# Kernel tuning notes

Measured on AMD Instinct MI355X. Metric: run time of the kernel, lower is better.

## Reference

```python
import jax, jax.numpy as jnp
import numpy as np

B, T = 16, 256
SD, AD = 24, 8
K = SD + AD           # in_dim
H = 1                 # num_heads
HD1, HD2 = 256, 256


def setup_inputs() -> dict:
    key = jax.random.key(0)
    ks = jax.random.split(key, 16)
    p = lambda kk, shp, s=0.05: jax.random.normal(kk, shp, dtype=jnp.float32) * s
    inp = {
        "state": jax.random.normal(ks[0], (B, T, SD), dtype=jnp.float32),
        "action": jax.random.normal(ks[1], (B, T, AD), dtype=jnp.float32),
        "Wq": p(ks[2], (H * K, K)), "bq": p(ks[3], (H * K,)),
        "Wk": p(ks[4], (H * K, K)), "bk": p(ks[5], (H * K,)),
        "Wv": p(ks[6], (H * K, K)), "bv": p(ks[7], (H * K,)),
        "W1": p(ks[8], (HD1, H * K + K)), "b1": p(ks[9], (HD1,)),
        "W2": p(ks[10], (HD2, HD1)), "b2": p(ks[11], (HD2,)),
        # out layer init_layer_uniform(-0.003, 0.003)
        "Wout": jax.random.uniform(ks[12], (1, HD1), minval=-0.003, maxval=0.003, dtype=jnp.float32),
        "bout": jax.random.uniform(ks[13], (1,), minval=-0.003, maxval=0.003, dtype=jnp.float32),
    }
    return inp


def reference(state, action, Wq, bq, Wk, bk, Wv, bv, W1, b1, W2, b2, Wout, bout):
    s = jnp.concatenate([state, action], axis=-1)            # (b,t,k)
    b, t, k = s.shape
    h = H
    # rel[b,i,j,:] = s[b,j] - s[b,i]
    rel = s[:, None, :, :] - s[:, :, None, :]                # (b,t,t,k)
    q = jax.nn.relu(jnp.einsum('btk,nk->btn', s, Wq) + bq).reshape(b, t, h, k)
    kk = jax.nn.relu(jnp.einsum('bijk,nk->bijn', rel, Wk) + bk).reshape(b, t, t, h, k)
    vv = jax.nn.relu(jnp.einsum('bijk,nk->bijn', rel, Wv) + bv).reshape(b, t, t, h, k)
    scores = jnp.einsum('bijhk,bihk->bhij', kk, q) / jnp.sqrt(jnp.float32(k))
    w = jax.nn.softmax(scores, axis=-1)                      # softmax over j
    x = jnp.einsum('bhij,bijhk->bihk', w, vv).reshape(b, t, h * k)
    x = jnp.concatenate([x, s], axis=-1)                     # (b,t,h*k+k)
    x = jax.nn.relu(jnp.einsum('btn,mn->btm', x, W1) + b1)
    x = jax.nn.relu(jnp.einsum('btn,mn->btm', x, W2) + b2)
    value = jnp.einsum('btn,mn->btm', x, Wout) + bout        # (b,t,1)
    return value
```

## Files before the change

kernel.cpp:

```cpp
#include <hip/hip_runtime.h>

#define NB 16
#define NT 256
#define NK 32
#define NROWS (NB * NT)
static constexpr float INV_SQRT_K = 0.17677669529663687f;

__global__ __launch_bounds__(256) void prep_kernel(
    const float* __restrict__ state, const float* __restrict__ action,
    const float* __restrict__ Wq, const float* __restrict__ bq,
    const float* __restrict__ Wk, const float* __restrict__ Wv,
    float* __restrict__ q, float* __restrict__ Ks, float* __restrict__ Vs,
    float* __restrict__ xcat)
{
    __shared__ float s_sh[8][32];
    const int tid = threadIdx.x;
    const int r = tid >> 5, n = tid & 31;
    const int row = blockIdx.x * 8 + r;
    float sval = (n < 24) ? state[row * 24 + n] : action[row * 8 + (n - 24)];
    s_sh[r][n] = sval;
    __syncthreads();
    float aq = 0.f, ak = 0.f, av = 0.f;
#pragma unroll
    for (int k = 0; k < 32; ++k) {
        float sv = s_sh[r][k];
        aq = fmaf(sv, Wq[n * 32 + k], aq);
        ak = fmaf(sv, Wk[n * 32 + k], ak);
        av = fmaf(sv, Wv[n * 32 + k], av);
    }
    q[row * 32 + n]  = fmaxf(aq + bq[n], 0.f);
    Ks[row * 32 + n] = ak;
    Vs[row * 32 + n] = av;
    xcat[row * 64 + 32 + n] = sval;
}

__global__ __launch_bounds__(256) void attn_kernel(
    const float* __restrict__ q, const float* __restrict__ Ks,
    const float* __restrict__ Vs, const float* __restrict__ bk,
    const float* __restrict__ bv, float* __restrict__ xcat)
{
    __shared__ float Ki[32], Vi[32], qi[32], bks[32], bvs[32];
    __shared__ float sc[256];
    __shared__ float wred[4];
    __shared__ float part[8][32];
    const int tid = threadIdx.x;
    const int b = blockIdx.x >> 8, i = blockIdx.x & 255;
    const int ibase = (b * 256 + i) * 32;
    if (tid < 32) {
        Ki[tid]  = Ks[ibase + tid];
        Vi[tid]  = Vs[ibase + tid];
        qi[tid]  = q[ibase + tid];
        bks[tid] = bk[tid];
        bvs[tid] = bv[tid];
    }
    __syncthreads();

    const int j = tid;
    const float* kp = Ks + (b * 256 + j) * 32;
    float acc = 0.f;
#pragma unroll
    for (int k = 0; k < 32; ++k) {
        float kkv = fmaxf(kp[k] - Ki[k] + bks[k], 0.f);
        acc = fmaf(kkv, qi[k], acc);
    }
    const float sval = acc * INV_SQRT_K;

    float m = sval;
#pragma unroll
    for (int off = 32; off >= 1; off >>= 1) m = fmaxf(m, __shfl_xor(m, off));
    if ((tid & 63) == 0) wred[tid >> 6] = m;
    __syncthreads();
    m = fmaxf(fmaxf(wred[0], wred[1]), fmaxf(wred[2], wred[3]));
    const float e = expf(sval - m);
    float ssum = e;
#pragma unroll
    for (int off = 32; off >= 1; off >>= 1) ssum += __shfl_xor(ssum, off);
    __syncthreads();
    if ((tid & 63) == 0) wred[tid >> 6] = ssum;
    __syncthreads();
    const float tot = (wred[0] + wred[1]) + (wred[2] + wred[3]);
    sc[j] = e / tot;
    __syncthreads();

    const int k = tid & 31, g = tid >> 5;
    const float* vp = Vs + (b * 256 + g * 32) * 32;
    const float vi = Vi[k], bvk = bvs[k];
    float xacc = 0.f;
#pragma unroll
    for (int jj = 0; jj < 32; ++jj) {
        float vv = fmaxf(vp[jj * 32 + k] - vi + bvk, 0.f);
        xacc = fmaf(sc[g * 32 + jj], vv, xacc);
    }
    part[g][k] = xacc;
    __syncthreads();
    if (tid < 32) {
        float x = 0.f;
#pragma unroll
        for (int gg = 0; gg < 8; ++gg) x += part[gg][tid];
        xcat[(b * 256 + i) * 64 + tid] = x;
    }
}

__global__ __launch_bounds__(256) void mlp_kernel(
    const float* __restrict__ xcat,
    const float* __restrict__ W1, const float* __restrict__ b1,
    const float* __restrict__ W2, const float* __restrict__ b2,
    const float* __restrict__ Wout, const float* __restrict__ bout,
    float* __restrict__ out)
{
    __shared__ float xc[8][64];
    __shared__ float h1[8][256];
    __shared__ float h2[8][256];
    const int tid = threadIdx.x;
    const int row0 = blockIdx.x * 8;

    ((float*)xc)[tid]       = xcat[row0 * 64 + tid];
    ((float*)xc)[tid + 256] = xcat[row0 * 64 + tid + 256];
    __syncthreads();

    const int m = tid;
    float acc[8];
#pragma unroll
    for (int r = 0; r < 8; ++r) acc[r] = 0.f;
    const float* w1p = W1 + m * 64;
#pragma unroll 8
    for (int n = 0; n < 64; ++n) {
        float w = w1p[n];
#pragma unroll
        for (int r = 0; r < 8; ++r) acc[r] = fmaf(w, xc[r][n], acc[r]);
    }
    float bb = b1[m];
#pragma unroll
    for (int r = 0; r < 8; ++r) h1[r][m] = fmaxf(acc[r] + bb, 0.f);
    __syncthreads();

#pragma unroll
    for (int r = 0; r < 8; ++r) acc[r] = 0.f;
    const float* w2p = W2 + m * 256;
#pragma unroll 4
    for (int n = 0; n < 256; ++n) {
        float w = w2p[n];
#pragma unroll
        for (int r = 0; r < 8; ++r) acc[r] = fmaf(w, h1[r][n], acc[r]);
    }
    bb = b2[m];
#pragma unroll
    for (int r = 0; r < 8; ++r) h2[r][m] = fmaxf(acc[r] + bb, 0.f);
    __syncthreads();

    if (tid < 128) {
        const int r = tid >> 4, l = tid & 15;
        float a = 0.f;
        for (int n = l; n < 256; n += 16) a = fmaf(h2[r][n], Wout[n], a);
#pragma unroll
        for (int mm = 8; mm >= 1; mm >>= 1) a += __shfl_xor(a, mm);
        if (l == 0) out[row0 + r] = a + bout[0];
    }
}

extern "C" void kernel_launch(void* const* d_in, const int* in_sizes, int n_in,
                              void* d_out, int out_size, void* d_ws, size_t ws_size,
                              hipStream_t stream)
{
    const float* state  = (const float*)d_in[0];
    const float* action = (const float*)d_in[1];
    const float* Wq     = (const float*)d_in[2];
    const float* bq     = (const float*)d_in[3];
    const float* Wk     = (const float*)d_in[4];
    const float* bk     = (const float*)d_in[5];
    const float* Wv     = (const float*)d_in[6];
    const float* bv     = (const float*)d_in[7];
    const float* W1     = (const float*)d_in[8];
    const float* b1     = (const float*)d_in[9];
    const float* W2     = (const float*)d_in[10];
    const float* b2     = (const float*)d_in[11];
    const float* Wout   = (const float*)d_in[12];
    const float* bout   = (const float*)d_in[13];
    float* out = (float*)d_out;

    float* ws   = (float*)d_ws;
    float* q    = ws;
    float* Ks   = q  + NROWS * NK;
    float* Vs   = Ks + NROWS * NK;
    float* xcat = Vs + NROWS * NK;

    prep_kernel<<<NROWS / 8, 256, 0, stream>>>(state, action, Wq, bq, Wk, Wv,
                                               q, Ks, Vs, xcat);
    attn_kernel<<<NROWS, 256, 0, stream>>>(q, Ks, Vs, bk, bv, xcat);
    mlp_kernel<<<NROWS / 8, 256, 0, stream>>>(xcat, W1, b1, W2, b2, Wout, bout, out);
}
```

Before: 134.2 us.

## Process four query rows per attention block and fold biases into projections

The attention kernel now handles four query rows i per block, so each j-row of K and V loaded from global memory is reused across four queries. K rows are loaded with float4 into registers. The bias terms and the 1/sqrt(k) scale move into the prep kernel, which removes per-element adds in the inner loops. The softmax is restructured so each wave reduces one query row with shuffles only, dropping several block barriers. This uses more registers and shared memory per block and launches a quarter as many blocks.

```diff
diff --git a/kernel.cpp b/kernel.cpp
--- a/kernel.cpp
+++ b/kernel.cpp
@@ -4,13 +4,15 @@
 #define NT 256
 #define NK 32
 #define NROWS (NB * NT)
+#define GQ 4
 static constexpr float INV_SQRT_K = 0.17677669529663687f;
 
 __global__ __launch_bounds__(256) void prep_kernel(
     const float* __restrict__ state, const float* __restrict__ action,
     const float* __restrict__ Wq, const float* __restrict__ bq,
-    const float* __restrict__ Wk, const float* __restrict__ Wv,
-    float* __restrict__ q, float* __restrict__ Ks, float* __restrict__ Vs,
+    const float* __restrict__ Wk, const float* __restrict__ bk,
+    const float* __restrict__ Wv, const float* __restrict__ bv,
+    float* __restrict__ q, float* __restrict__ Ksb, float* __restrict__ Vsb,
     float* __restrict__ xcat)
 {
     __shared__ float s_sh[8][32];
@@ -28,76 +30,100 @@
         ak = fmaf(sv, Wk[n * 32 + k], ak);
         av = fmaf(sv, Wv[n * 32 + k], av);
     }
-    q[row * 32 + n]  = fmaxf(aq + bq[n], 0.f);
-    Ks[row * 32 + n] = ak;
-    Vs[row * 32 + n] = av;
+    q[row * 32 + n]   = fmaxf(aq + bq[n], 0.f) * INV_SQRT_K;
+    Ksb[row * 32 + n] = ak + bk[n];
+    Vsb[row * 32 + n] = av + bv[n];
     xcat[row * 64 + 32 + n] = sval;
 }
 
 __global__ __launch_bounds__(256) void attn_kernel(
-    const float* __restrict__ q, const float* __restrict__ Ks,
-    const float* __restrict__ Vs, const float* __restrict__ bk,
+    const float* __restrict__ q, const float* __restrict__ Ksb,
+    const float* __restrict__ Vsb, const float* __restrict__ bk,
     const float* __restrict__ bv, float* __restrict__ xcat)
 {
-    __shared__ float Ki[32], Vi[32], qi[32], bks[32], bvs[32];
-    __shared__ float sc[256];
-    __shared__ float wred[4];
-    __shared__ float part[8][32];
+    __shared__ float Kie[GQ][32];
+    __shared__ float Vie[GQ][32];
+    __shared__ float qi[GQ][32];
+    __shared__ float sc[GQ][256];
+    __shared__ float part[GQ][8][32];
     const int tid = threadIdx.x;
-    const int b = blockIdx.x >> 8, i = blockIdx.x & 255;
-    const int ibase = (b * 256 + i) * 32;
-    if (tid < 32) {
-        Ki[tid]  = Ks[ibase + tid];
-        Vi[tid]  = Vs[ibase + tid];
-        qi[tid]  = q[ibase + tid];
-        bks[tid] = bk[tid];
-        bvs[tid] = bv[tid];
+    const int b  = blockIdx.x >> 6;
+    const int i0 = (blockIdx.x & 63) << 2;
+    const int rowbase = b * 256;
+
+    {
+        const int g = (tid >> 5) & 3, k = tid & 31;
+        const int ib = (rowbase + i0 + g) * 32 + k;
+        if (tid < 128) {
+            Kie[g][k] = Ksb[ib] - bk[k];
+            qi[g][k]  = q[ib];
+        } else {
+            Vie[g][k] = Vsb[ib] - bv[k];
+        }
     }
     __syncthreads();
 
     const int j = tid;
-    const float* kp = Ks + (b * 256 + j) * 32;
-    float acc = 0.f;
+    const float4* kp4 = (const float4*)(Ksb + (rowbase + j) * 32);
+    float kr[32];
+#pragma unroll
+    for (int u = 0; u < 8; ++u) {
+        float4 v = kp4[u];
+        kr[u * 4 + 0] = v.x; kr[u * 4 + 1] = v.y;
+        kr[u * 4 + 2] = v.z; kr[u * 4 + 3] = v.w;
+    }
+    float acc[GQ] = {0.f, 0.f, 0.f, 0.f};
 #pragma unroll
     for (int k = 0; k < 32; ++k) {
-        float kkv = fmaxf(kp[k] - Ki[k] + bks[k], 0.f);
-        acc = fmaf(kkv, qi[k], acc);
-    }
-    const float sval = acc * INV_SQRT_K;
-
-    float m = sval;
-#pragma unroll
-    for (int off = 32; off >= 1; off >>= 1) m = fmaxf(m, __shfl_xor(m, off));
-    if ((tid & 63) == 0) wred[tid >> 6] = m;
-    __syncthreads();
-    m = fmaxf(fmaxf(wred[0], wred[1]), fmaxf(wred[2], wred[3]));
-    const float e = expf(sval - m);
-    float ssum = e;
-#pragma unroll
-    for (int off = 32; off >= 1; off >>= 1) ssum += __shfl_xor(ssum, off);
-    __syncthreads();
-    if ((tid & 63) == 0) wred[tid >> 6] = ssum;
-    __syncthreads();
-    const float tot = (wred[0] + wred[1]) + (wred[2] + wred[3]);
-    sc[j] = e / tot;
-    __syncthreads();
-
-    const int k = tid & 31, g = tid >> 5;
-    const float* vp = Vs + (b * 256 + g * 32) * 32;
-    const float vi = Vi[k], bvk = bvs[k];
-    float xacc = 0.f;
-#pragma unroll
-    for (int jj = 0; jj < 32; ++jj) {
-        float vv = fmaxf(vp[jj * 32 + k] - vi + bvk, 0.f);
-        xacc = fmaf(sc[g * 32 + jj], vv, xacc);
-    }
-    part[g][k] = xacc;
-    __syncthreads();
-    if (tid < 32) {
+        float kv = kr[k];
+#pragma unroll
+        for (int g = 0; g < GQ; ++g)
+            acc[g] = fmaf(fmaxf(kv - Kie[g][k], 0.f), qi[g][k], acc[g]);
+    }
+#pragma unroll
+    for (int g = 0; g < GQ; ++g) sc[g][j] = acc[g];
+    __syncthreads();
+
+    {
+        const int g = tid >> 6, l = tid & 63;
+        float e0 = sc[g][l], e1 = sc[g][l + 64], e2 = sc[g][l + 128], e3 = sc[g][l + 192];
+        float m = fmaxf(fmaxf(e0, e1), fmaxf(e2, e3));
+#pragma unroll
+        for (int off = 32; off >= 1; off >>= 1) m = fmaxf(m, __shfl_xor(m, off));
+        e0 = expf(e0 - m); e1 = expf(e1 - m); e2 = expf(e2 - m); e3 = expf(e3 - m);
+        float ssum = ((e0 + e1) + (e2 + e3));
+#pragma unroll
+        for (int off = 32; off >= 1; off >>= 1) ssum += __shfl_xor(ssum, off);
+        float inv = 1.f / ssum;
+        sc[g][l] = e0 * inv; sc[g][l + 64] = e1 * inv;
+        sc[g][l + 128] = e2 * inv; sc[g][l + 192] = e3 * inv;
+    }
+    __syncthreads();
+
+    {
+        const int k = tid & 31, grp = tid >> 5;
+        const float* vp = Vsb + (rowbase + grp * 32) * 32;
+        float vie[GQ];
+#pragma unroll
+        for (int g = 0; g < GQ; ++g) vie[g] = Vie[g][k];
+        float xacc[GQ] = {0.f, 0.f, 0.f, 0.f};
+#pragma unroll
+        for (int jj = 0; jj < 32; ++jj) {
+            float v = vp[jj * 32 + k];
+#pragma unroll
+            for (int g = 0; g < GQ; ++g)
+                xacc[g] = fmaf(sc[g][grp * 32 + jj], fmaxf(v - vie[g], 0.f), xacc[g]);
+        }
+#pragma unroll
+        for (int g = 0; g < GQ; ++g) part[g][grp][k] = xacc[g];
+    }
+    __syncthreads();
+    if (tid < 128) {
+        const int g = tid >> 5, k = tid & 31;
         float x = 0.f;
 #pragma unroll
-        for (int gg = 0; gg < 8; ++gg) x += part[gg][tid];
-        xcat[(b * 256 + i) * 64 + tid] = x;
+        for (int gg = 0; gg < 8; ++gg) x += part[g][gg][k];
+        xcat[(rowbase + i0 + g) * 64 + k] = x;
     }
 }
 
@@ -180,12 +206,12 @@
 
     float* ws   = (float*)d_ws;
     float* q    = ws;
-    float* Ks   = q  + NROWS * NK;
-    float* Vs   = Ks + NROWS * NK;
-    float* xcat = Vs + NROWS * NK;
-
-    prep_kernel<<<NROWS / 8, 256, 0, stream>>>(state, action, Wq, bq, Wk, Wv,
-                                               q, Ks, Vs, xcat);
-    attn_kernel<<<NROWS, 256, 0, stream>>>(q, Ks, Vs, bk, bv, xcat);
+    float* Ksb  = q   + NROWS * NK;
+    float* Vsb  = Ksb + NROWS * NK;
+    float* xcat = Vsb + NROWS * NK;
+
+    prep_kernel<<<NROWS / 8, 256, 0, stream>>>(state, action, Wq, bq, Wk, bk,
+                                               Wv, bv, q, Ksb, Vsb, xcat);
+    attn_kernel<<<NROWS / GQ, 256, 0, stream>>>(q, Ksb, Vsb, bk, bv, xcat);
     mlp_kernel<<<NROWS / 8, 256, 0, stream>>>(xcat, W1, b1, W2, b2, Wout, bout, out);
 }
```

Result: faster. 122.6 us (-8.7%).
